# Kernel tuning notes

Hardware: AMD Instinct MI355X
Metric: run time of the kernel (lower is better)

Reference implementation:

```python
import jax, jax.numpy as jnp
import numpy as np

N = 100000        # nodes
E = 1600000       # edges (before self-loops)
IN = 128          # in_dim
HID = 16          # hidden_dim per head
HEADS = 8
OUT = 40          # out_dim (classes)
BN_EPS = 1e-5
NEG_SLOPE = 0.2


def setup_inputs() -> dict:
    key = jax.random.key(0)
    ks = jax.random.split(key, 16)
    s = 0.05
    return {
        "x": jax.random.normal(ks[0], (N, IN), dtype=jnp.float32),
        "edge_index": jax.random.randint(ks[1], (2, E), 0, N, dtype=jnp.int64),
        "W1": jax.random.normal(ks[2], (IN, HEADS * HID), dtype=jnp.float32) * s,
        "att_src1": jax.random.normal(ks[3], (HEADS, HID), dtype=jnp.float32) * s,
        "att_dst1": jax.random.normal(ks[4], (HEADS, HID), dtype=jnp.float32) * s,
        "bias1": jax.random.normal(ks[5], (HEADS * HID,), dtype=jnp.float32) * s,
        "bn_gamma": 1.0 + jax.random.normal(ks[6], (HEADS * HID,), dtype=jnp.float32) * 0.1,
        "bn_beta": jax.random.normal(ks[7], (HEADS * HID,), dtype=jnp.float32) * 0.1,
        "bn_mean": jax.random.normal(ks[8], (HEADS * HID,), dtype=jnp.float32) * 0.1,
        "bn_var": jax.random.uniform(ks[9], (HEADS * HID,), dtype=jnp.float32, minval=0.5, maxval=1.5),
        "W2": jax.random.normal(ks[10], (HEADS * HID, OUT), dtype=jnp.float32) * s,
        "att_src2": jax.random.normal(ks[11], (1, OUT), dtype=jnp.float32) * s,
        "att_dst2": jax.random.normal(ks[12], (1, OUT), dtype=jnp.float32) * s,
        "bias2": jax.random.normal(ks[13], (OUT,), dtype=jnp.float32) * s,
        "W_skip": jax.random.normal(ks[14], (IN, HEADS * HID), dtype=jnp.float32) * s,
        "b_skip": jax.random.normal(ks[15], (HEADS * HID,), dtype=jnp.float32) * s,
    }


def gat_conv(x, src, dst, W, a_src, a_dst, bias, heads, ch, concat):
    """PyG GATConv (eval mode): per-edge attention, segment softmax over dst, scatter-add."""
    n = x.shape[0]
    h = (x @ W).reshape(n, heads, ch)                      # [N,H,C]
    alpha_s = jnp.einsum("nhc,hc->nh", h, a_src)            # [N,H]
    alpha_d = jnp.einsum("nhc,hc->nh", h, a_dst)            # [N,H]
    e = jax.nn.leaky_relu(alpha_s[src] + alpha_d[dst], NEG_SLOPE)   # [E,H]
    # numerically stable segment softmax over destination node
    m = jax.ops.segment_max(e, dst, num_segments=n)          # [N,H]
    ex = jnp.exp(e - m[dst])                                 # [E,H]
    denom = jax.ops.segment_sum(ex, dst, num_segments=n)     # [N,H]
    alpha = ex / (denom[dst] + 1e-16)                        # [E,H]
    out = jax.ops.segment_sum(alpha[:, :, None] * h[src], dst, num_segments=n)  # [N,H,C]
    out = out.reshape(n, heads * ch) if concat else out.mean(axis=1)
    return out + bias


def reference(x, edge_index, W1, att_src1, att_dst1, bias1,
              bn_gamma, bn_beta, bn_mean, bn_var,
              W2, att_src2, att_dst2, bias2, W_skip, b_skip):
    n = x.shape[0]
    # add self-loops (PyG GATConv default)
    loops = jnp.arange(n, dtype=edge_index.dtype)
    src = jnp.concatenate([edge_index[0], loops])
    dst = jnp.concatenate([edge_index[1], loops])

    identity = x @ W_skip + b_skip                           # skip projection

    h = gat_conv(x, src, dst, W1, att_src1, att_dst1, bias1, HEADS, HID, True)
    h = (h - bn_mean) * (bn_gamma / jnp.sqrt(bn_var + BN_EPS)) + bn_beta  # BN eval
    h = jax.nn.elu(h)                                        # dropout: eval no-op
    h = h + identity

    att_s2 = att_src2  # [1,OUT] heads=1
    out = gat_conv(h, src, dst, W2, att_s2, att_dst2, bias2, 1, OUT, False)
    return jax.nn.log_softmax(out, axis=1)
```

## Files before the change

kernel.cpp:

```cpp
#include <hip/hip_runtime.h>
#include <math.h>

#define NEG_SLOPE 0.2f
#define BN_EPS 1e-5f
#define BSH 9
#define BMASK 511
#define LOG2E 1.44269504088896f
#define BCAP 12288

typedef __attribute__((ext_vector_type(8))) short short8;
typedef __attribute__((ext_vector_type(4))) float f32x4;

__device__ __forceinline__ float wave_max64(float v) {
  #pragma unroll
  for (int o = 32; o; o >>= 1) v = fmaxf(v, __shfl_xor(v, o, 64));
  return v;
}
__device__ __forceinline__ float wave_sum64(float v) {
  #pragma unroll
  for (int o = 32; o; o >>= 1) v += __shfl_xor(v, o, 64);
  return v;
}

__device__ __forceinline__ unsigned pack2bf(float a, float b) {
  unsigned ua = __float_as_uint(a);
  unsigned ub = __float_as_uint(b);
  ua = ua + 0x7fffu + ((ua >> 16) & 1u);
  ub = ub + 0x7fffu + ((ub >> 16) & 1u);
  return (ua >> 16) | (ub & 0xffff0000u);
}
__device__ __forceinline__ float bf_lo(unsigned u) { return __uint_as_float(u << 16); }
__device__ __forceinline__ float bf_hi(unsigned u) { return __uint_as_float(u & 0xffff0000u); }

union U8 { short8 s; uint4 u; };

__global__ void prep_kernel(const float* __restrict__ W1,
                            const float* __restrict__ att_s,
                            const float* __restrict__ att_d,
                            float* __restrict__ Mext,
                            const float* __restrict__ W2,
                            const float* __restrict__ att_s2,
                            const float* __restrict__ att_d2,
                            float* __restrict__ M2ext)
{
  int k = threadIdx.x;
  #pragma unroll
  for (int h = 0; h < 8; ++h) {
    float s = 0.f, d = 0.f;
    #pragma unroll
    for (int c = 0; c < 16; ++c) {
      float w = W1[k * 128 + h * 16 + c];
      s += w * att_s[h * 16 + c];
      d += w * att_d[h * 16 + c];
    }
    Mext[k * 16 + h] = s * LOG2E;
    Mext[k * 16 + 8 + h] = d * LOG2E;
  }
  float s2 = 0.f, d2 = 0.f;
  #pragma unroll
  for (int c = 0; c < 40; ++c) {
    float w = W2[k * 40 + c];
    s2 += w * att_s2[c];
    d2 += w * att_d2[c];
  }
  M2ext[k * 2] = s2 * LOG2E;
  M2ext[k * 2 + 1] = d2 * LOG2E;
}

__global__ __launch_bounds__(256) void gemm1_scatter_kernel(
    const float* __restrict__ X, const float* __restrict__ W1,
    const float* __restrict__ Wsk, const float* __restrict__ bsk,
    const float* __restrict__ Mext,
    unsigned short* __restrict__ h1f8, unsigned* __restrict__ identb,
    float* __restrict__ alpha_s, float* __restrict__ alpha_d, int N,
    const int* __restrict__ esrc, const int* __restrict__ edst,
    int* __restrict__ bcur, unsigned* __restrict__ pkbuf,
    int E, int T, int chunk, int NB, int G1)
{
  __shared__ uint4 Asm4[2048];
  const int t = threadIdx.x;

  if ((int)blockIdx.x >= G1) {
    int* hist  = (int*)Asm4;
    int* lbase = hist + 256;
    int* lcur  = hist + 512;
    const int bid = (int)blockIdx.x - G1;
    hist[t] = 0;
    __syncthreads();
    int s0 = bid * chunk;
    int s1 = min(s0 + chunk, T);
    for (int i = s0 + t; i < s1; i += 256) {
      int d = (i < E) ? edst[i] : (i - E);
      atomicAdd(&hist[d >> BSH], 1);
    }
    __syncthreads();
    if (t < NB) {
      int h = hist[t];
      lbase[t] = t * BCAP + (h ? atomicAdd(&bcur[t], h) : 0);
      lcur[t] = 0;
    }
    __syncthreads();
    for (int i = s0 + t; i < s1; i += 256) {
      int d, s;
      if (i < E) { d = edst[i]; s = esrc[i]; } else { d = s = i - E; }
      int b = d >> BSH;
      int p = lbase[b] + atomicAdd(&lcur[b], 1);
      pkbuf[p] = ((unsigned)(d & BMASK) << 17) | (unsigned)s;
    }
    return;
  }

  const int l = t & 63, wave = t >> 6;
  const int lx = l & 15, ly = l >> 4;
  const int row0 = blockIdx.x * 128;
  const int wn0 = wave * 64;

  short8 b[4][4];
  short8 b4[4] = {};
  #pragma unroll
  for (int nf = 0; nf < 4; ++nf) {
    int c = wn0 + nf * 16 + lx;
    const float* bp = (c < 128) ? (W1 + c) : (Wsk + c - 128);
    #pragma unroll
    for (int kf = 0; kf < 4; ++kf) {
      int k0 = kf * 32 + ly * 8;
      U8 f;
      f.u.x = pack2bf(bp[(k0 + 0) * 128], bp[(k0 + 1) * 128]);
      f.u.y = pack2bf(bp[(k0 + 2) * 128], bp[(k0 + 3) * 128]);
      f.u.z = pack2bf(bp[(k0 + 4) * 128], bp[(k0 + 5) * 128]);
      f.u.w = pack2bf(bp[(k0 + 6) * 128], bp[(k0 + 7) * 128]);
      b[nf][kf] = f.s;
    }
  }
  if (wave == 0) {
    const float* bp = Mext + lx;
    #pragma unroll
    for (int kf = 0; kf < 4; ++kf) {
      int k0 = kf * 32 + ly * 8;
      U8 f;
      f.u.x = pack2bf(bp[(k0 + 0) * 16], bp[(k0 + 1) * 16]);
      f.u.y = pack2bf(bp[(k0 + 2) * 16], bp[(k0 + 3) * 16]);
      f.u.z = pack2bf(bp[(k0 + 4) * 16], bp[(k0 + 5) * 16]);
      f.u.w = pack2bf(bp[(k0 + 6) * 16], bp[(k0 + 7) * 16]);
      b4[kf] = f.s;
    }
  }

  {
    int rl = t >> 1;
    int half = t & 1;
    int r = row0 + rl;
    const float* xp = X + (size_t)r * 128 + half * 64;
    #pragma unroll
    for (int i = 0; i < 8; ++i) {
      float4 f0 = make_float4(0.f, 0.f, 0.f, 0.f), f1 = f0;
      if (r < N) {
        f0 = *(const float4*)(xp + i * 8);
        f1 = *(const float4*)(xp + i * 8 + 4);
      }
      uint4 u;
      u.x = pack2bf(f0.x, f0.y); u.y = pack2bf(f0.z, f0.w);
      u.z = pack2bf(f1.x, f1.y); u.w = pack2bf(f1.z, f1.w);
      int woff = (rl * 256 + half * 128 + i * 16) ^ ((rl & 7) << 4);
      *(uint4*)((char*)Asm4 + woff) = u;
    }
  }
  __syncthreads();

  float bval[4];
  if (wave >= 2) {
    #pragma unroll
    for (int nf = 0; nf < 4; ++nf) bval[nf] = bsk[(wave - 2) * 64 + nf * 16 + lx];
  }

  for (int mf = 0; mf < 8; ++mf) {
    short8 a[4];
    int rowl = mf * 16 + lx;
    #pragma unroll
    for (int kf = 0; kf < 4; ++kf)
      a[kf] = *(short8*)((char*)Asm4 + ((rowl * 256 + kf * 64 + ly * 16) ^ ((lx & 7) << 4)));

    int rbase = row0 + mf * 16 + ly * 4;

    #pragma unroll
    for (int nf = 0; nf < 4; ++nf) {
      f32x4 acc = {0.f, 0.f, 0.f, 0.f};
      #pragma unroll
      for (int kf = 0; kf < 4; ++kf)
        acc = __builtin_amdgcn_mfma_f32_16x16x32_bf16(a[kf], b[nf][kf], acc, 0, 0, 0);
      if (wave < 2) {
        int c = wn0 + nf * 16 + lx;
        #pragma unroll
        for (int reg = 0; reg < 4; ++reg) {
          float v = acc[reg];
          float vp = __shfl_xor(v, 1, 64);
          int r = rbase + reg;
          if (!(lx & 1) && r < N) {
            int u = __builtin_amdgcn_cvt_pk_fp8_f32(v, vp, 0, false);
            *(unsigned short*)((char*)h1f8 + (unsigned)r * 128u + (unsigned)c) =
                (unsigned short)u;
          }
        }
      } else {
        int c = (wave - 2) * 64 + nf * 16 + lx;
        #pragma unroll
        for (int reg = 0; reg < 4; ++reg) {
          float v = acc[reg] + bval[nf];
          float vp = __shfl_xor(v, 1, 64);
          int r = rbase + reg;
          if (!(lx & 1) && r < N)
            identb[(unsigned)r * 64u + (unsigned)(c >> 1)] = pack2bf(v, vp);
        }
      }
    }

    if (wave == 0) {
      f32x4 acc = {0.f, 0.f, 0.f, 0.f};
      #pragma unroll
      for (int kf = 0; kf < 4; ++kf)
        acc = __builtin_amdgcn_mfma_f32_16x16x32_bf16(a[kf], b4[kf], acc, 0, 0, 0);
      #pragma unroll
      for (int reg = 0; reg < 4; ++reg) {
        int r = rbase + reg;
        if (r < N) {
          if (lx < 8) alpha_s[(size_t)r * 8 + lx] = acc[reg];
          else        alpha_d[(size_t)r * 8 + (lx - 8)] = acc[reg];
        }
      }
    }
  }
}

__global__ __launch_bounds__(256) void passB_kernel(
    const unsigned* __restrict__ pkbuf, const int* __restrict__ bcnt,
    int* __restrict__ starts, int* __restrict__ ends,
    int* __restrict__ ssrc, int N)
{
  __shared__ int cnt[512];
  __shared__ int ps[256];
  __shared__ int cur[512];
  const int t = threadIdx.x;
  const int b = blockIdx.x;
  const int bs = b * BCAP;
  const int be = bs + bcnt[b];

  cnt[t] = 0; cnt[t + 256] = 0;
  __syncthreads();
  for (int i = bs + t; i < be; i += 256)
    atomicAdd(&cnt[pkbuf[i] >> 17], 1);
  __syncthreads();

  int a = cnt[2 * t], b2 = cnt[2 * t + 1];
  ps[t] = a + b2;
  __syncthreads();
  for (int d = 1; d < 256; d <<= 1) {
    int u = (t >= d) ? ps[t - d] : 0;
    __syncthreads();
    ps[t] += u;
    __syncthreads();
  }
  int excl = ps[t] - (a + b2);
  cur[2 * t] = excl;
  cur[2 * t + 1] = excl + a;
  __syncthreads();

  const int node0 = b << BSH;
  {
    int n0 = node0 + 2 * t, n1 = node0 + 2 * t + 1;
    if (n0 < N) { starts[n0] = bs + cur[2 * t];     ends[n0] = bs + cur[2 * t] + a; }
    if (n1 < N) { starts[n1] = bs + cur[2 * t + 1]; ends[n1] = bs + cur[2 * t + 1] + b2; }
  }
  __syncthreads();

  for (int i = bs + t; i < be; i += 256) {
    unsigned pk = pkbuf[i];
    int d = pk >> 17;
    int p = atomicAdd(&cur[d], 1);
    ssrc[bs + p] = (int)(pk & 0x1FFFFu);
  }
}

__global__ __launch_bounds__(256) void agg1_kernel(
    const int* __restrict__ starts, const int* __restrict__ ends,
    const int* __restrict__ ssrc,
    const float* __restrict__ as1, const float* __restrict__ ad1,
    const unsigned short* __restrict__ h1f8,
    const float* __restrict__ bias1, const float* __restrict__ gamma,
    const float* __restrict__ beta, const float* __restrict__ mean,
    const float* __restrict__ var,
    const unsigned* __restrict__ identb, unsigned* __restrict__ hpostb, int N)
{
  const int w = threadIdx.x >> 6, l = threadIdx.x & 63;
  const int n = blockIdx.x * 4 + w;
  if (n >= N) return;
  const int e8 = l >> 3;
  const int hh = l & 7;
  const int h2_4 = (l >> 3) * 4;
  const int c0 = l * 2;
  const unsigned l2 = (unsigned)(l * 2);
  const float adp = ad1[(unsigned)n * 8u + (unsigned)hh];
  const int jb = starts[n], je = ends[n];

  const float bb0 = bias1[c0], bb1 = bias1[c0 + 1];
  const float sc0 = gamma[c0] * rsqrtf(var[c0] + BN_EPS);
  const float sc1 = gamma[c0 + 1] * rsqrtf(var[c0 + 1] + BN_EPS);
  const float mn0 = mean[c0], mn1 = mean[c0 + 1];
  const float bt0 = beta[c0], bt1 = beta[c0 + 1];

  const char* h1c = (const char*)h1f8;

  float dsum = 0.f, a0 = 0.f, a1 = 0.f;

#define PHASE2(K, SVEC, EW) { \
    unsigned sk = (unsigned)__builtin_amdgcn_readlane(SVEC, (K) * 8); \
    float ewk = __uint_as_float( \
        __builtin_amdgcn_ds_bpermute(h2_4 + (K) * 32, __float_as_uint(EW))); \
    unsigned u8 = *(const unsigned short*)(h1c + ((size_t)sk << 7) + l2); \
    a0 += ewk * __builtin_amdgcn_cvt_f32_fp8(u8, 0); \
    a1 += ewk * __builtin_amdgcn_cvt_f32_fp8(u8, 1); }

  int j = jb;
  for (; j + 16 <= je; j += 16) {
    int sv0 = ssrc[j + e8];
    int sv1 = ssrc[j + 8 + e8];
    float e0 = as1[(unsigned)sv0 * 8u + (unsigned)hh] + adp;
    e0 = fmaxf(e0, NEG_SLOPE * e0);
    float ew0 = exp2f(e0);
    float e1 = as1[(unsigned)sv1 * 8u + (unsigned)hh] + adp;
    e1 = fmaxf(e1, NEG_SLOPE * e1);
    float ew1 = exp2f(e1);
    dsum += ew0 + ew1;
    PHASE2(0, sv0, ew0) PHASE2(1, sv0, ew0) PHASE2(2, sv0, ew0) PHASE2(3, sv0, ew0)
    PHASE2(4, sv0, ew0) PHASE2(5, sv0, ew0) PHASE2(6, sv0, ew0) PHASE2(7, sv0, ew0)
    PHASE2(0, sv1, ew1) PHASE2(1, sv1, ew1) PHASE2(2, sv1, ew1) PHASE2(3, sv1, ew1)
    PHASE2(4, sv1, ew1) PHASE2(5, sv1, ew1) PHASE2(6, sv1, ew1) PHASE2(7, sv1, ew1)
  }
  for (; j + 8 <= je; j += 8) {
    int svec = ssrc[j + e8];
    float e = as1[(unsigned)svec * 8u + (unsigned)hh] + adp;
    e = fmaxf(e, NEG_SLOPE * e);
    float ew = exp2f(e);
    dsum += ew;
    PHASE2(0, svec, ew) PHASE2(1, svec, ew) PHASE2(2, svec, ew) PHASE2(3, svec, ew)
    PHASE2(4, svec, ew) PHASE2(5, svec, ew) PHASE2(6, svec, ew) PHASE2(7, svec, ew)
  }
  int rem = je - j;
  if (rem > 0) {
    int jj = j + (e8 < rem ? e8 : 0);
    int svec = ssrc[jj];
    float e = as1[(unsigned)svec * 8u + (unsigned)hh] + adp;
    e = fmaxf(e, NEG_SLOPE * e);
    float ew = (e8 < rem) ? exp2f(e) : 0.f;
    dsum += ew;
    for (int k = 0; k < rem; ++k) {
      unsigned sk = (unsigned)__builtin_amdgcn_readlane(svec, k * 8);
      float ewk = __uint_as_float(
          __builtin_amdgcn_ds_bpermute(h2_4 + (k << 5), __float_as_uint(ew)));
      unsigned u8 = *(const unsigned short*)(h1c + ((size_t)sk << 7) + l2);
      a0 += ewk * __builtin_amdgcn_cvt_f32_fp8(u8, 0);
      a1 += ewk * __builtin_amdgcn_cvt_f32_fp8(u8, 1);
    }
  }
#undef PHASE2

  dsum += __shfl_xor(dsum, 8, 64);
  dsum += __shfl_xor(dsum, 16, 64);
  dsum += __shfl_xor(dsum, 32, 64);
  float denom = __uint_as_float(
      __builtin_amdgcn_ds_bpermute(h2_4, __float_as_uint(dsum)));

  float inv = 1.f / (denom + 1e-16f);
  unsigned uid = identb[(unsigned)n * 64u + (unsigned)l];
  float o0 = a0 * inv + bb0;
  float o1 = a1 * inv + bb1;
  o0 = (o0 - mn0) * sc0 + bt0;
  o1 = (o1 - mn1) * sc1 + bt1;
  o0 = o0 > 0.f ? o0 : expm1f(o0);
  o1 = o1 > 0.f ? o1 : expm1f(o1);
  o0 += bf_lo(uid); o1 += bf_hi(uid);
  hpostb[(unsigned)n * 64u + (unsigned)l] = pack2bf(o0, o1);
}

__global__ __launch_bounds__(256) void gemm2_kernel(
    const unsigned* __restrict__ hpostb, const float* __restrict__ W2,
    const float* __restrict__ M2ext,
    unsigned* __restrict__ h2b, float* __restrict__ as2, float* __restrict__ ad2, int N)
{
  const int t = threadIdx.x;
  const int l = t & 63, wave = t >> 6;
  const int lx = l & 15, ly = l >> 4;
  const int row0 = blockIdx.x * 128;

  short8 b[3][4];
  short8 b4[4];
  {
    #pragma unroll
    for (int nf = 0; nf < 3; ++nf) {
      int col = nf * 16 + lx;
      bool v = col < 40;
      const float* bp = W2 + (v ? col : 0);
      #pragma unroll
      for (int kf = 0; kf < 4; ++kf) {
        int k0 = kf * 32 + ly * 8;
        U8 f;
        if (v) {
          f.u.x = pack2bf(bp[(k0 + 0) * 40], bp[(k0 + 1) * 40]);
          f.u.y = pack2bf(bp[(k0 + 2) * 40], bp[(k0 + 3) * 40]);
          f.u.z = pack2bf(bp[(k0 + 4) * 40], bp[(k0 + 5) * 40]);
          f.u.w = pack2bf(bp[(k0 + 6) * 40], bp[(k0 + 7) * 40]);
        } else {
          f.u = make_uint4(0, 0, 0, 0);
        }
        b[nf][kf] = f.s;
      }
    }
    bool va = lx < 2;
    const float* bp = M2ext + (va ? lx : 0);
    #pragma unroll
    for (int kf = 0; kf < 4; ++kf) {
      int k0 = kf * 32 + ly * 8;
      U8 f;
      if (va) {
        f.u.x = pack2bf(bp[(k0 + 0) * 2], bp[(k0 + 1) * 2]);
        f.u.y = pack2bf(bp[(k0 + 2) * 2], bp[(k0 + 3) * 2]);
        f.u.z = pack2bf(bp[(k0 + 4) * 2], bp[(k0 + 5) * 2]);
        f.u.w = pack2bf(bp[(k0 + 6) * 2], bp[(k0 + 7) * 2]);
      } else {
        f.u = make_uint4(0, 0, 0, 0);
      }
      b4[kf] = f.s;
    }
  }

  #pragma unroll
  for (int i2 = 0; i2 < 2; ++i2) {
    int mf = wave * 2 + i2;
    int arow = row0 + mf * 16 + lx;
    short8 a[4];
    #pragma unroll
    for (int kf = 0; kf < 4; ++kf) {
      U8 f;
      f.u = make_uint4(0, 0, 0, 0);
      if (arow < N)
        f.u = *(const uint4*)(hpostb + (unsigned)arow * 64u + (unsigned)(kf * 16 + ly * 4));
      a[kf] = f.s;
    }

    int rbase = row0 + mf * 16 + ly * 4;

    #pragma unroll
    for (int nf = 0; nf < 3; ++nf) {
      f32x4 acc = {0.f, 0.f, 0.f, 0.f};
      #pragma unroll
      for (int kf = 0; kf < 4; ++kf)
        acc = __builtin_amdgcn_mfma_f32_16x16x32_bf16(a[kf], b[nf][kf], acc, 0, 0, 0);
      int c = nf * 16 + lx;
      #pragma unroll
      for (int reg = 0; reg < 4; ++reg) {
        float v = acc[reg];
        float vp = __shfl_xor(v, 1, 64);
        int r = rbase + reg;
        if (r < N && c < 40 && !(lx & 1))
          h2b[((unsigned)r << 5) + (unsigned)(c >> 1)] = pack2bf(v, vp);
      }
    }
    {
      f32x4 acc = {0.f, 0.f, 0.f, 0.f};
      #pragma unroll
      for (int kf = 0; kf < 4; ++kf)
        acc = __builtin_amdgcn_mfma_f32_16x16x32_bf16(a[kf], b4[kf], acc, 0, 0, 0);
      #pragma unroll
      for (int reg = 0; reg < 4; ++reg) {
        int r = rbase + reg;
        if (r < N) {
          if (lx == 0) as2[r] = acc[reg];
          else if (lx == 1) ad2[r] = acc[reg];
        }
      }
    }
  }
}

__global__ __launch_bounds__(256) void agg2_kernel(
    const int* __restrict__ starts, const int* __restrict__ ends,
    const int* __restrict__ ssrc,
    const float* __restrict__ as2, const float* __restrict__ ad2,
    const unsigned* __restrict__ h2b, const float* __restrict__ bias2,
    float* __restrict__ outp, int N)
{
  const int w = threadIdx.x >> 6, l = threadIdx.x & 63;
  const int n = blockIdx.x * 4 + w;
  if (n >= N) return;
  const int g = l / 20;
  const int cl = l - g * 20;
  const unsigned cl4 = (unsigned)(cl * 4);
  const bool act = l < 60;
  const float ad = ad2[n];
  const int jb = starts[n], je = ends[n];

  const char* as2c = (const char*)as2;
  const char* h2c = (const char*)h2b;

  float denom = 0.f, a0 = 0.f, a1 = 0.f;

#define EDGE2(JJ, GUARD) { \
    bool v = act && (GUARD); \
    unsigned s = v ? (unsigned)ssrc[JJ] : 0u; \
    float e = *(const float*)(as2c + (s << 2)) + ad; \
    e = fmaxf(e, NEG_SLOPE * e); \
    float ex = v ? exp2f(e) : 0.f; \
    unsigned u = *(const unsigned*)(h2c + ((size_t)s << 7) + cl4); \
    denom += ex; \
    a0 += ex * bf_lo(u); \
    a1 += ex * bf_hi(u); }

  int j = jb;
  for (; j + 9 <= je; j += 9) {
    EDGE2(j + g, true)
    EDGE2(j + 3 + g, true)
    EDGE2(j + 6 + g, true)
  }
  for (; j < je; j += 3) {
    EDGE2(j + g, (j + g) < je)
  }
#undef EDGE2

  a0 += __shfl(a0, l + 20, 64) + __shfl(a0, l + 40, 64);
  a1 += __shfl(a1, l + 20, 64) + __shfl(a1, l + 40, 64);
  denom += __shfl(denom, l + 20, 64) + __shfl(denom, l + 40, 64);

  const int lc = l < 20 ? l : 0;
  float inv = 1.f / (denom + 1e-16f);
  float o0 = a0 * inv + bias2[2 * lc];
  float o1 = a1 * inv + bias2[2 * lc + 1];

  float mx = wave_max64(l < 20 ? fmaxf(o0, o1) : -3.4e38f);
  float se = wave_sum64(l < 20 ? __expf(o0 - mx) + __expf(o1 - mx) : 0.f);
  float ls = logf(se);
  if (l < 20)
    *(float2*)&outp[(size_t)n * 40 + 2 * l] = make_float2(o0 - mx - ls, o1 - mx - ls);
}

extern "C" void kernel_launch(void* const* d_in, const int* in_sizes, int n_in,
                              void* d_out, int out_size, void* d_ws, size_t ws_size,
                              hipStream_t stream)
{
  const float* x        = (const float*)d_in[0];
  const int*   ei       = (const int*)d_in[1];
  const float* W1       = (const float*)d_in[2];
  const float* att_src1 = (const float*)d_in[3];
  const float* att_dst1 = (const float*)d_in[4];
  const float* bias1    = (const float*)d_in[5];
  const float* bn_gamma = (const float*)d_in[6];
  const float* bn_beta  = (const float*)d_in[7];
  const float* bn_mean  = (const float*)d_in[8];
  const float* bn_var   = (const float*)d_in[9];
  const float* W2       = (const float*)d_in[10];
  const float* att_src2 = (const float*)d_in[11];
  const float* att_dst2 = (const float*)d_in[12];
  const float* bias2    = (const float*)d_in[13];
  const float* W_skip   = (const float*)d_in[14];
  const float* b_skip   = (const float*)d_in[15];

  const int N = in_sizes[0] / 128;
  const int E = in_sizes[1] / 2;
  const int T = E + N;
  const int NB = (N + BMASK) >> BSH;

  char* p = (char*)d_ws;
  auto alloc = [&](size_t bytes) { char* q = p; p += (bytes + 255) & ~255ull; return q; };
  unsigned short* h1f8 = (unsigned short*)alloc((size_t)N * 128);
  unsigned* hpostb = (unsigned*)alloc((size_t)N * 64 * 4);
  unsigned* identb = (unsigned*)alloc((size_t)N * 64 * 4);
  float* as1     = (float*)alloc((size_t)N * 8 * 4);
  float* ad1     = (float*)alloc((size_t)N * 8 * 4);
  float* Mext    = (float*)alloc(128 * 16 * 4);
  float* M2ext   = (float*)alloc(128 * 2 * 4);
  int*   starts  = (int*)alloc((size_t)N * 4);
  int*   ends    = (int*)alloc((size_t)N * 4);
  unsigned* pkbuf= (unsigned*)alloc((size_t)NB * BCAP * 4);
  int*   ssrc    = (int*)alloc((size_t)NB * BCAP * 4);
  int*   bcur    = (int*)alloc((size_t)NB * 4);
  unsigned* h2b = (unsigned*)h1f8;
  float* as2 = as1;
  float* ad2 = ad1;

  const int* ei_src = ei;
  const int* ei_dst = ei + E;

  hipMemsetAsync(bcur, 0, (size_t)NB * 4, stream);

  prep_kernel<<<1, 128, 0, stream>>>(W1, att_src1, att_dst1, Mext,
                                     W2, att_src2, att_dst2, M2ext);

  const int G1 = (N + 127) / 128;
  const int NBLK_A = 512;
  const int chunk = (T + NBLK_A - 1) / NBLK_A;
  gemm1_scatter_kernel<<<G1 + NBLK_A, 256, 0, stream>>>(
      x, W1, W_skip, b_skip, Mext, h1f8, identb, as1, ad1, N,
      ei_src, ei_dst, bcur, pkbuf, E, T, chunk, NB, G1);

  passB_kernel<<<NB, 256, 0, stream>>>(pkbuf, bcur, starts, ends, ssrc, N);

  agg1_kernel<<<(N + 3) / 4, 256, 0, stream>>>(starts, ends, ssrc, as1, ad1, h1f8,
                                               bias1, bn_gamma, bn_beta, bn_mean, bn_var,
                                               identb, hpostb, N);
  gemm2_kernel<<<(N + 127) / 128, 256, 0, stream>>>(hpostb, W2, M2ext,
                                                    h2b, as2, ad2, N);
  agg2_kernel<<<(N + 3) / 4, 256, 0, stream>>>(starts, ends, ssrc, as2, ad2, h2b, bias2,
                                               (float*)d_out, N);
}
```

Before: 258.4 us.

## Split layer-2 features into two dense arrays and drop 16-edge unroll in agg1

```diff
diff --git a/kernel.cpp b/kernel.cpp
--- a/kernel.cpp
+++ b/kernel.cpp
@@ -320,21 +320,6 @@
     a1 += ewk * __builtin_amdgcn_cvt_f32_fp8(u8, 1); }
 
   int j = jb;
-  for (; j + 16 <= je; j += 16) {
-    int sv0 = ssrc[j + e8];
-    int sv1 = ssrc[j + 8 + e8];
-    float e0 = as1[(unsigned)sv0 * 8u + (unsigned)hh] + adp;
-    e0 = fmaxf(e0, NEG_SLOPE * e0);
-    float ew0 = exp2f(e0);
-    float e1 = as1[(unsigned)sv1 * 8u + (unsigned)hh] + adp;
-    e1 = fmaxf(e1, NEG_SLOPE * e1);
-    float ew1 = exp2f(e1);
-    dsum += ew0 + ew1;
-    PHASE2(0, sv0, ew0) PHASE2(1, sv0, ew0) PHASE2(2, sv0, ew0) PHASE2(3, sv0, ew0)
-    PHASE2(4, sv0, ew0) PHASE2(5, sv0, ew0) PHASE2(6, sv0, ew0) PHASE2(7, sv0, ew0)
-    PHASE2(0, sv1, ew1) PHASE2(1, sv1, ew1) PHASE2(2, sv1, ew1) PHASE2(3, sv1, ew1)
-    PHASE2(4, sv1, ew1) PHASE2(5, sv1, ew1) PHASE2(6, sv1, ew1) PHASE2(7, sv1, ew1)
-  }
   for (; j + 8 <= je; j += 8) {
     int svec = ssrc[j + e8];
     float e = as1[(unsigned)svec * 8u + (unsigned)hh] + adp;
@@ -384,7 +369,8 @@
 __global__ __launch_bounds__(256) void gemm2_kernel(
     const unsigned* __restrict__ hpostb, const float* __restrict__ W2,
     const float* __restrict__ M2ext,
-    unsigned* __restrict__ h2b, float* __restrict__ as2, float* __restrict__ ad2, int N)
+    unsigned* __restrict__ h2a, unsigned* __restrict__ h2b2,
+    float* __restrict__ as2, float* __restrict__ ad2, int N)
 {
   const int t = threadIdx.x;
   const int l = t & 63, wave = t >> 6;
@@ -455,13 +441,17 @@
       for (int kf = 0; kf < 4; ++kf)
         acc = __builtin_amdgcn_mfma_f32_16x16x32_bf16(a[kf], b[nf][kf], acc, 0, 0, 0);
       int c = nf * 16 + lx;
+      int cp = c >> 1;
       #pragma unroll
       for (int reg = 0; reg < 4; ++reg) {
         float v = acc[reg];
         float vp = __shfl_xor(v, 1, 64);
         int r = rbase + reg;
-        if (r < N && c < 40 && !(lx & 1))
-          h2b[((unsigned)r << 5) + (unsigned)(c >> 1)] = pack2bf(v, vp);
+        if (r < N && c < 40 && !(lx & 1)) {
+          unsigned pk = pack2bf(v, vp);
+          if (cp < 16) h2a[((unsigned)r << 4) + (unsigned)cp] = pk;
+          else         h2b2[((unsigned)r << 2) + (unsigned)(cp - 16)] = pk;
+        }
       }
     }
     {
@@ -485,7 +475,8 @@
     const int* __restrict__ starts, const int* __restrict__ ends,
     const int* __restrict__ ssrc,
     const float* __restrict__ as2, const float* __restrict__ ad2,
-    const unsigned* __restrict__ h2b, const float* __restrict__ bias2,
+    const unsigned* __restrict__ h2a, const unsigned* __restrict__ h2b2,
+    const float* __restrict__ bias2,
     float* __restrict__ outp, int N)
 {
   const int w = threadIdx.x >> 6, l = threadIdx.x & 63;
@@ -493,13 +484,14 @@
   if (n >= N) return;
   const int g = l / 20;
   const int cl = l - g * 20;
-  const unsigned cl4 = (unsigned)(cl * 4);
   const bool act = l < 60;
   const float ad = ad2[n];
   const int jb = starts[n], je = ends[n];
 
+  const char* hbase = (cl < 16) ? ((const char*)h2a + (unsigned)cl * 4u)
+                                : ((const char*)h2b2 + (unsigned)(cl - 16) * 4u);
+  const unsigned hshift = (cl < 16) ? 6u : 4u;
   const char* as2c = (const char*)as2;
-  const char* h2c = (const char*)h2b;
 
   float denom = 0.f, a0 = 0.f, a1 = 0.f;
 
@@ -509,7 +501,7 @@
     float e = *(const float*)(as2c + (s << 2)) + ad; \
     e = fmaxf(e, NEG_SLOPE * e); \
     float ex = v ? exp2f(e) : 0.f; \
-    unsigned u = *(const unsigned*)(h2c + ((size_t)s << 7) + cl4); \
+    unsigned u = *(const unsigned*)(hbase + ((size_t)s << hshift)); \
     denom += ex; \
     a0 += ex * bf_lo(u); \
     a1 += ex * bf_hi(u); }
@@ -581,7 +573,8 @@
   unsigned* pkbuf= (unsigned*)alloc((size_t)NB * BCAP * 4);
   int*   ssrc    = (int*)alloc((size_t)NB * BCAP * 4);
   int*   bcur    = (int*)alloc((size_t)NB * 4);
-  unsigned* h2b = (unsigned*)h1f8;
+  unsigned* h2a  = (unsigned*)h1f8;
+  unsigned* h2b2 = (unsigned*)((char*)h1f8 + (size_t)N * 64);
   float* as2 = as1;
   float* ad2 = ad1;
 
@@ -606,7 +599,8 @@
                                                bias1, bn_gamma, bn_beta, bn_mean, bn_var,
                                                identb, hpostb, N);
   gemm2_kernel<<<(N + 127) / 128, 256, 0, stream>>>(hpostb, W2, M2ext,
-                                                    h2b, as2, ad2, N);
-  agg2_kernel<<<(N + 3) / 4, 256, 0, stream>>>(starts, ends, ssrc, as2, ad2, h2b, bias2,
+                                                    h2a, h2b2, as2, ad2, N);
+  agg2_kernel<<<(N + 3) / 4, 256, 0, stream>>>(starts, ends, ssrc, as2, ad2,
+                                               h2a, h2b2, bias2,
                                                (float*)d_out, N);
 }
```

New measurement: 248.9 us. 3.7% less time.
